# Kernel tuning notes

Hardware: AMD Instinct MI355X
Metric: run time of the kernel (lower is better)

## Reference

```python
import jax, jax.numpy as jnp
import numpy as np
from jax import lax

N = 64          # padded / uniform graph size
B = 512         # number of graph pairs
E = 512         # edges per graph
GCN_SIZES = [64, 32, 16]
CONV_OUT = [8, 16, 32]
D_IN = 16


def gcn_conv(x, src, dst, W, b):
    # PyG GCNConv: add self-loops, symmetric norm D^-1/2 (A+I) D^-1/2, then XW + b
    n = x.shape[0]
    h = x @ W
    deg = jnp.zeros((n,), x.dtype).at[dst].add(1.0) + 1.0  # +1 self-loop
    dinv = lax.rsqrt(deg)
    msg = h[src] * (dinv[src] * dinv[dst])[:, None]
    agg = jnp.zeros_like(h).at[dst].add(msg) + h * (dinv * dinv)[:, None]
    return agg + b


def gcn_pass(x, ei, Ws, bs):
    src, dst = ei[0], ei[1]
    feats = []
    h = x
    for i in range(len(Ws)):
        h = gcn_conv(h, src, dst, Ws[i], bs[i])
        feats.append(h)               # pre-ReLU features are used for similarity
        if i < len(Ws) - 1:
            h = jax.nn.relu(h)        # dropout p used in eval -> identity
    return feats


def conv_same(x, w, b):
    y = lax.conv_general_dilated(x, w, (1, 1), 'SAME',
                                 dimension_numbers=('NCHW', 'OIHW', 'NCHW'))
    return y + b[None, :, None, None]


def maxpool2(x):
    return lax.reduce_window(x, -jnp.inf, lax.max, (1, 1, 2, 2), (1, 1, 2, 2), 'VALID')


def setup_inputs() -> dict:
    key = jax.random.key(0)
    ks = jax.random.split(key, 32)
    f32 = jnp.float32
    x_q = jax.random.normal(ks[0], (B * N, D_IN), f32)
    x_c = jax.random.normal(ks[1], (B * N, D_IN), f32)
    off = (jnp.arange(B, dtype=jnp.int32) * N)[:, None]
    eq_s = (jax.random.randint(ks[2], (B, E), 0, N, jnp.int32) + off).reshape(-1)
    eq_d = (jax.random.randint(ks[3], (B, E), 0, N, jnp.int32) + off).reshape(-1)
    ec_s = (jax.random.randint(ks[4], (B, E), 0, N, jnp.int32) + off).reshape(-1)
    ec_d = (jax.random.randint(ks[5], (B, E), 0, N, jnp.int32) + off).reshape(-1)
    edge_q = jnp.stack([eq_s, eq_d])
    edge_c = jnp.stack([ec_s, ec_d])

    def lin(k, fi, fo):
        return jax.random.normal(k, (fi, fo), f32) / np.sqrt(fi)

    inp = dict(x_q=x_q, x_c=x_c, edge_q=edge_q, edge_c=edge_c)
    dims = [D_IN] + GCN_SIZES
    for i in range(3):
        inp[f'gcn_w{i+1}'] = lin(ks[6 + i], dims[i], dims[i + 1])
        inp[f'gcn_b{i+1}'] = jnp.zeros((dims[i + 1],), f32)
    cin = [1] + CONV_OUT[:-1]
    for i in range(3):
        fan = cin[i] * 25
        inp[f'conv_w{i+1}'] = jax.random.normal(ks[10 + i], (3, CONV_OUT[i], cin[i], 5, 5), f32) / np.sqrt(fan)
        inp[f'conv_b{i+1}'] = jnp.zeros((3, CONV_OUT[i]), f32)
    inp['lin_w1'] = lin(ks[14], 6144, 256)
    inp['lin_b1'] = jnp.zeros((256,), f32)
    inp['lin_w2'] = lin(ks[15], 256, 16)
    inp['lin_b2'] = jnp.zeros((16,), f32)
    inp['score_w'] = lin(ks[16], 16, 1)
    inp['score_b'] = jnp.zeros((1,), f32)
    return inp


def _forward(x_q, x_c, gcn_w1, gcn_b1, gcn_w2, gcn_b2, gcn_w3, gcn_b3,
             conv_w1, conv_b1, conv_w2, conv_b2, conv_w3, conv_b3,
             lin_w1, lin_b1, lin_w2, lin_b2, score_w, score_b,
             edge_q, edge_c):
    Ws = (gcn_w1, gcn_w2, gcn_w3)
    bs = (gcn_b1, gcn_b2, gcn_b3)
    qf = gcn_pass(x_q, edge_q, Ws, bs)   # list of [B*N, d_i]
    cf = gcn_pass(x_c, edge_c, Ws, bs)
    sims = [jnp.einsum('bnd,bmd->bnm', q.reshape(B, N, -1), c.reshape(B, N, -1))
            for q, c in zip(qf, cf)]
    cw = (conv_w1, conv_w2, conv_w3)
    cb = (conv_b1, conv_b2, conv_b3)
    outs = []
    for m in range(3):                    # separate conv weights per similarity matrix
        z = sims[m][:, None]              # [B, 1, N, N]
        for l in range(3):
            z = maxpool2(jax.nn.relu(conv_same(z, cw[l][m], cb[l][m])))
        outs.append(z)                    # [B, 32, 8, 8]
    feat = jnp.concatenate(outs, axis=1).reshape(B, 6144)
    h = jax.nn.relu(feat @ lin_w1 + lin_b1)
    h = jax.nn.relu(h @ lin_w2 + lin_b2)
    return (h @ score_w + score_b).reshape(-1)  # is_sig=False -> logits [B]


def reference(x_q, x_c, edge_q, edge_c, gcn_w1, gcn_b1, gcn_w2, gcn_b2, gcn_w3, gcn_b3,
              conv_w1, conv_b1, conv_w2, conv_b2, conv_w3, conv_b3,
              lin_w1, lin_b1, lin_w2, lin_b2, score_w, score_b):
    return _forward(x_q, x_c, gcn_w1, gcn_b1, gcn_w2, gcn_b2, gcn_w3, gcn_b3,
                    conv_w1, conv_b1, conv_w2, conv_b2, conv_w3, conv_b3,
                    lin_w1, lin_b1, lin_w2, lin_b2, score_w, score_b,
                    edge_q, edge_c)
```

## Files before the change

kernel.cpp:

```cpp
#include <hip/hip_runtime.h>
#include <hip/hip_bf16.h>

constexpr int B = 512, N = 64, E = 512, NE = B * E;

typedef __attribute__((ext_vector_type(8))) short bf8v;
typedef __attribute__((ext_vector_type(4))) float f32x4;
typedef unsigned short u16;

__device__ __forceinline__ u16 f2bf(float f) {
  unsigned u = __builtin_bit_cast(unsigned, f);
  u += 0x7FFFu + ((u >> 16) & 1u);
  return (u16)(u >> 16);
}

__device__ __forceinline__ int cmin(int a, int b) { return a < b ? a : b; }

template <int DIN, int DOUT, int NR, int NC, bool STORE_NEXT>
__device__ __forceinline__ void gcn_layer(
    float* __restrict__ At, float* __restrict__ Xt, float* __restrict__ Hs,
    const float* __restrict__ W, const float* __restrict__ bias,
    u16* __restrict__ fout, int g, int t) {
  constexpr int XS = 68;
  constexpr int CT = DOUT / NC;
  static_assert((64 / NR) * CT == 512, "thread mapping");
  const int ct = t % CT, nt = t / CT;
  const int n0 = NR * nt, c0 = NC * ct;
  {
    float acc[NR][NC] = {};
#pragma unroll 4
    for (int k = 0; k < DIN; ++k) {
      float xa[NR];
      if constexpr (NR == 4) {
        float4 xv = *(const float4*)&Xt[k * XS + n0];
        xa[0] = xv.x; xa[1] = xv.y; xa[2] = xv.z; xa[3] = xv.w;
      } else {
        float2 xv = *(const float2*)&Xt[k * XS + n0];
        xa[0] = xv.x; xa[1] = xv.y;
      }
      float wa[NC];
      if constexpr (NC == 2) {
        float2 wv = *(const float2*)&W[k * DOUT + c0];
        wa[0] = wv.x; wa[1] = wv.y;
      } else {
        wa[0] = W[k * DOUT + c0];
      }
#pragma unroll
      for (int i = 0; i < NR; ++i)
#pragma unroll
        for (int j = 0; j < NC; ++j) acc[i][j] += xa[i] * wa[j];
    }
#pragma unroll
    for (int i = 0; i < NR; ++i) {
      if constexpr (NC == 2)
        *(float2*)&Hs[(n0 + i) * XS + c0] = make_float2(acc[i][0], acc[i][1]);
      else
        Hs[(n0 + i) * XS + c0] = acc[i][0];
    }
  }
  __syncthreads();
  {
    float acc[NR][NC] = {};
#pragma unroll 4
    for (int s = 0; s < N; ++s) {
      float aa[NR];
      if constexpr (NR == 4) {
        float4 av = *(const float4*)&At[s * XS + n0];
        aa[0] = av.x; aa[1] = av.y; aa[2] = av.z; aa[3] = av.w;
      } else {
        float2 av = *(const float2*)&At[s * XS + n0];
        aa[0] = av.x; aa[1] = av.y;
      }
      float ha[NC];
      if constexpr (NC == 2) {
        float2 hv = *(const float2*)&Hs[s * XS + c0];
        ha[0] = hv.x; ha[1] = hv.y;
      } else {
        ha[0] = Hs[s * XS + c0];
      }
#pragma unroll
      for (int i = 0; i < NR; ++i)
#pragma unroll
        for (int j = 0; j < NC; ++j) acc[i][j] += aa[i] * ha[j];
    }
    float bv[NC];
#pragma unroll
    for (int j = 0; j < NC; ++j) bv[j] = bias[c0 + j];
#pragma unroll
    for (int i = 0; i < NR; ++i) {
      float st[NC];
#pragma unroll
      for (int j = 0; j < NC; ++j) st[j] = acc[i][j] + bv[j];
      if constexpr (NC == 2) {
        unsigned pack = (unsigned)f2bf(st[0]) | ((unsigned)f2bf(st[1]) << 16);
        *(unsigned*)&fout[(size_t)g * N * DOUT + (size_t)(n0 + i) * DOUT + c0] = pack;
      } else {
        fout[(size_t)g * N * DOUT + (size_t)(n0 + i) * DOUT + c0] = f2bf(st[0]);
      }
      if (STORE_NEXT) {
#pragma unroll
        for (int j = 0; j < NC; ++j)
          Xt[(c0 + j) * XS + n0 + i] = fmaxf(st[j], 0.f);
      }
    }
  }
  __syncthreads();
}

__global__ __launch_bounds__(512) void gcn_fused(
    const float* __restrict__ xq, const float* __restrict__ xc,
    const float* __restrict__ W1, const float* __restrict__ b1,
    const float* __restrict__ W2, const float* __restrict__ b2,
    const float* __restrict__ W3, const float* __restrict__ b3,
    const int* __restrict__ eq, const int* __restrict__ ec,
    u16* __restrict__ f1q, u16* __restrict__ f1c,
    u16* __restrict__ f2q, u16* __restrict__ f2c,
    u16* __restrict__ f3q, u16* __restrict__ f3c) {
  constexpr int XS = 68;
  __shared__ __align__(16) float At[N * XS];
  __shared__ __align__(16) float Xt[N * XS];
  __shared__ __align__(16) float Hs[N * XS];
  __shared__ float dl[N];
  __shared__ int cnt[N];
  const int g = blockIdx.x, t = threadIdx.x;
  const float* x = blockIdx.y ? xc : xq;
  const int* edges = blockIdx.y ? ec : eq;
  u16* o1 = blockIdx.y ? f1c : f1q;
  u16* o2 = blockIdx.y ? f2c : f2q;
  u16* o3 = blockIdx.y ? f3c : f3q;
  for (int i = t; i < N * 16; i += 512) {
    int n = i / 16, k = i % 16;
    Xt[k * XS + n] = x[(size_t)g * N * 16 + i];
  }
  for (int i = t; i < N * XS; i += 512) At[i] = 0.f;
  if (t < N) cnt[t] = 1;
  __syncthreads();
  const int* srcp = edges + (size_t)g * E;
  const int* dstp = edges + NE + (size_t)g * E;
  for (int j = t; j < E; j += 512) atomicAdd(&cnt[dstp[j] & 63], 1);
  __syncthreads();
  if (t < N) dl[t] = rsqrtf((float)cnt[t]);
  __syncthreads();
  for (int j = t; j < E; j += 512) {
    int s = srcp[j] & 63, d = dstp[j] & 63;
    atomicAdd(&At[s * XS + d], dl[s] * dl[d]);
  }
  if (t < N) atomicAdd(&At[t * XS + t], dl[t] * dl[t]);
  __syncthreads();
  gcn_layer<16, 64, 4, 2, true>(At, Xt, Hs, W1, b1, o1, g, t);
  gcn_layer<64, 32, 4, 1, true>(At, Xt, Hs, W2, b2, o2, g, t);
  gcn_layer<32, 16, 2, 1, false>(At, Xt, Hs, W3, b3, o3, g, t);
}

__global__ __launch_bounds__(256, 4) void simconv1(
    const u16* __restrict__ f1q, const u16* __restrict__ f1c,
    const u16* __restrict__ f2q, const u16* __restrict__ f2c,
    const u16* __restrict__ f3q, const u16* __restrict__ f3c,
    const float* __restrict__ w, const float* __restrict__ bias,
    u16* __restrict__ out) {
  constexpr int PS = 68, QS = 72;
  __shared__ __align__(16) u16 Qs[64 * QS];
  __shared__ __align__(16) u16 Cs[64 * QS];
  __shared__ __align__(16) float simp[68 * 68];
  __shared__ float wls[25 * 8];
  __shared__ float bls[8];
  const int b = blockIdx.x, m = blockIdx.y, t = threadIdx.x;
  for (int i = t; i < 68 * 68; i += 256) simp[i] = 0.f;
  if (t < 200) {
    int oc = t / 25, tap = t % 25;
    wls[tap * 8 + oc] = w[m * 200 + t];
  }
  if (t < 8) bls[t] = bias[m * 8 + t];
  const u16* fq = (m == 0) ? f1q : (m == 1) ? f2q : f3q;
  const u16* fc = (m == 0) ? f1c : (m == 1) ? f2c : f3c;
  const int D = 64 >> m;
  const int SEG = D >> 3;
  for (int i = t; i < 64 * SEG; i += 256) {
    int n = i / SEG, s = i - n * SEG;
    *(uint4*)&Qs[n * QS + s * 8] = *(const uint4*)&fq[(size_t)b * 64 * D + n * D + s * 8];
    *(uint4*)&Cs[n * QS + s * 8] = *(const uint4*)&fc[(size_t)b * 64 * D + n * D + s * 8];
  }
  if (m == 2 && t < 128) {
    int n = t >> 1, s = t & 1;
    uint4 z = {0u, 0u, 0u, 0u};
    *(uint4*)&Qs[n * QS + 16 + s * 8] = z;
    *(uint4*)&Cs[n * QS + 16 + s * 8] = z;
  }
  __syncthreads();
  const int w4 = t >> 6, lane = t & 63;
  const int r16 = lane & 15, kg = lane >> 4;
  const int Kpad = (m == 0) ? 64 : 32;
#pragma unroll 1
  for (int ct = 0; ct < 4; ++ct) {
    f32x4 acc = {0.f, 0.f, 0.f, 0.f};
    for (int ks = 0; ks < Kpad; ks += 32) {
      bf8v a = *(const bf8v*)&Qs[(w4 * 16 + r16) * QS + ks + kg * 8];
      bf8v bb = *(const bf8v*)&Cs[(ct * 16 + r16) * QS + ks + kg * 8];
      acc = __builtin_amdgcn_mfma_f32_16x16x32_bf16(a, bb, acc, 0, 0, 0);
    }
#pragma unroll
    for (int j = 0; j < 4; ++j)
      simp[(w4 * 16 + kg * 4 + j + 2) * PS + ct * 16 + r16 + 2] = acc[j];
  }
  __syncthreads();
  const int gy = t >> 4, gx = t & 15;
  float pr[8][8];
#pragma unroll
  for (int yy = 0; yy < 8; ++yy) {
    float4 a = *(const float4*)&simp[(4 * gy + yy) * PS + 4 * gx];
    float4 bb = *(const float4*)&simp[(4 * gy + yy) * PS + 4 * gx + 4];
    pr[yy][0] = a.x; pr[yy][1] = a.y; pr[yy][2] = a.z; pr[yy][3] = a.w;
    pr[yy][4] = bb.x; pr[yy][5] = bb.y; pr[yy][6] = bb.z; pr[yy][7] = bb.w;
  }
  u16* op = out + (size_t)(b * 3 + m) * 8192;
#pragma unroll 1
  for (int p2 = 0; p2 < 4; ++p2) {
    float acc[2][16];
#pragma unroll
    for (int p = 0; p < 16; ++p) { acc[0][p] = 0.f; acc[1][p] = 0.f; }
#pragma unroll
    for (int ky = 0; ky < 5; ++ky)
#pragma unroll
      for (int kx = 0; kx < 5; ++kx) {
        float2 wv = *(const float2*)&wls[(ky * 5 + kx) * 8 + p2 * 2];
#pragma unroll
        for (int dy = 0; dy < 4; ++dy)
#pragma unroll
          for (int dx = 0; dx < 4; ++dx) {
            float rv = pr[ky + dy][kx + dx];
            acc[0][dy * 4 + dx] += rv * wv.x;
            acc[1][dy * 4 + dx] += rv * wv.y;
          }
      }
    float b0 = bls[p2 * 2], b1 = bls[p2 * 2 + 1];
#pragma unroll
    for (int ay = 0; ay < 2; ++ay)
#pragma unroll
      for (int ax = 0; ax < 2; ++ax) {
        float v0 = fmaxf(fmaxf(acc[0][(2 * ay) * 4 + 2 * ax], acc[0][(2 * ay) * 4 + 2 * ax + 1]),
                         fmaxf(acc[0][(2 * ay + 1) * 4 + 2 * ax], acc[0][(2 * ay + 1) * 4 + 2 * ax + 1]));
        float v1 = fmaxf(fmaxf(acc[1][(2 * ay) * 4 + 2 * ax], acc[1][(2 * ay) * 4 + 2 * ax + 1]),
                         fmaxf(acc[1][(2 * ay + 1) * 4 + 2 * ax], acc[1][(2 * ay + 1) * 4 + 2 * ax + 1]));
        v0 = fmaxf(v0 + b0, 0.f);
        v1 = fmaxf(v1 + b1, 0.f);
        unsigned pack = (unsigned)f2bf(v0) | ((unsigned)f2bf(v1) << 16);
        *(unsigned*)&op[(size_t)(((2 * gy + ay) * 32) + (2 * gx + ax)) * 8 + p2 * 2] = pack;
      }
  }
}

__global__ __launch_bounds__(256) void prep_kernel(
    const float* __restrict__ lw1, const float* __restrict__ cw2,
    const float* __restrict__ cw3, u16* __restrict__ wT,
    u16* __restrict__ w2p, u16* __restrict__ w3p) {
  const int t = threadIdx.x;
  if (blockIdx.x < 384) {
    __shared__ float tile[64][65];
    const int k0 = (blockIdx.x % 96) * 64, c0 = (blockIdx.x / 96) * 64;
    for (int i = t; i < 4096; i += 256) {
      int r = i >> 6, c = i & 63;
      tile[r][c] = lw1[(size_t)(k0 + r) * 256 + c0 + c];
    }
    __syncthreads();
    for (int i = t; i < 4096; i += 256) {
      int c = i >> 6, k = i & 63;
      wT[(size_t)(c0 + c) * 6144 + k0 + k] = f2bf(tile[k][c]);
    }
    return;
  }
  int i = (blockIdx.x - 384) * 256 + t;
  if (i < 3 * 7 * 16 * 40) {
    int m = i / 4480, r = i % 4480;
    int k = r % 40, rest = r / 40, oc = rest & 15, st = rest >> 4;
    u16 v = 0;
    if (k < 32) {
      int sl = k >> 3, ci = k & 7, tap = st * 4 + sl;
      if (tap < 25) v = f2bf(cw2[((size_t)(m * 16 + oc) * 8 + ci) * 25 + tap]);
    }
    w2p[i] = v;
  }
  if (i < 3 * 26 * 16 * 40) {
    int m = i / 16640, r = i % 16640;
    int k = r % 40, rest = r / 40, oc16 = rest & 15, sthalf = rest >> 4;
    int half = sthalf & 1, st = sthalf >> 1;
    u16 v = 0;
    if (k < 32) {
      int sl = k >> 4, ci = k & 15, tap = st * 2 + sl;
      int oc = half * 16 + oc16;
      if (tap < 25) v = f2bf(cw3[((size_t)(m * 32 + oc) * 16 + ci) * 25 + tap]);
    }
    w3p[i] = v;
  }
}

__global__ __launch_bounds__(256) void conv2_mfma(
    const u16* __restrict__ in, const u16* __restrict__ w2p,
    const float* __restrict__ bias, u16* __restrict__ out) {
  constexpr int PW = 36, BS = 40;
  __shared__ __align__(16) u16 ins[PW * PW * 8];
  __shared__ __align__(16) u16 wls[7 * 16 * BS];
  __shared__ float bls[16];
  const int b = blockIdx.x, m = blockIdx.y, t = threadIdx.x;
  const size_t ibase = (size_t)(b * 3 + m) * 8192;
  for (int i = t; i < PW * PW; i += 256) {
    int y = i / PW, x = i % PW;
    uint4 v = {0u, 0u, 0u, 0u};
    if (y >= 2 && y < 34 && x >= 2 && x < 34)
      v = *(const uint4*)&in[ibase + (size_t)((y - 2) * 32 + (x - 2)) * 8];
    *(uint4*)&ins[i * 8] = v;
  }
  {
    const u16* wsrc = w2p + m * 4480;
    for (int i = t; i < 560; i += 256) *(uint4*)&wls[i * 8] = *(const uint4*)&wsrc[i * 8];
  }
  if (t < 16) bls[t] = bias[m * 16 + t];
  __syncthreads();
  const int wv = t >> 6, lane = t & 63;
  const int oc = lane & 15, g = lane >> 4;
  const int xt = wv & 1, ypb = wv >> 1;
  const int x = xt * 16 + oc;
  const size_t obase = (size_t)(b * 3 + m) * 4096;
#pragma unroll 1
  for (int grp = 0; grp < 2; ++grp) {
    f32x4 acc[4][2];
#pragma unroll
    for (int i = 0; i < 4; ++i) {
      acc[i][0] = (f32x4){0.f, 0.f, 0.f, 0.f};
      acc[i][1] = (f32x4){0.f, 0.f, 0.f, 0.f};
    }
#pragma unroll
    for (int st = 0; st < 7; ++st) {
      bf8v bvv = *(const bf8v*)&wls[(st * 16 + oc) * BS + g * 8];
      const int c0 = cmin(st * 4 + 0, 24), c1 = cmin(st * 4 + 1, 24);
      const int c2 = cmin(st * 4 + 2, 24), c3 = cmin(st * 4 + 3, 24);
      const int k0 = (c0 / 5) * PW + c0 % 5, k1 = (c1 / 5) * PW + c1 % 5;
      const int k2 = (c2 / 5) * PW + c2 % 5, k3 = (c3 / 5) * PW + c3 % 5;
      const int koff = (g == 0) ? k0 : (g == 1) ? k1 : (g == 2) ? k2 : k3;
#pragma unroll
      for (int i = 0; i < 4; ++i) {
        const int y0 = 2 * ypb + 4 * (grp * 4 + i);
        const int abase = (y0 * PW + x + koff) * 8;
        bf8v a0 = *(const bf8v*)&ins[abase];
        acc[i][0] = __builtin_amdgcn_mfma_f32_16x16x32_bf16(a0, bvv, acc[i][0], 0, 0, 0);
        bf8v a1 = *(const bf8v*)&ins[abase + PW * 8];
        acc[i][1] = __builtin_amdgcn_mfma_f32_16x16x32_bf16(a1, bvv, acc[i][1], 0, 0, 0);
      }
    }
    const float bb = bls[oc];
#pragma unroll
    for (int i = 0; i < 4; ++i) {
      const int yp = ypb + 2 * (grp * 4 + i);
      const float v0 = fmaxf(fmaxf(fmaxf(acc[i][0][0], acc[i][0][1]),
                                   fmaxf(acc[i][1][0], acc[i][1][1])) + bb, 0.f);
      const float v1 = fmaxf(fmaxf(fmaxf(acc[i][0][2], acc[i][0][3]),
                                   fmaxf(acc[i][1][2], acc[i][1][3])) + bb, 0.f);
      const int px = xt * 8 + 2 * g;
      out[obase + (size_t)((yp * 16 + px) * 16 + oc)] = f2bf(v0);
      out[obase + (size_t)((yp * 16 + px + 1) * 16 + oc)] = f2bf(v1);
    }
  }
}

__global__ __launch_bounds__(256) void conv3_mfma(
    const u16* __restrict__ in, const u16* __restrict__ w3p,
    const float* __restrict__ bias, u16* __restrict__ feat) {
  constexpr int PW = 20, BS = 40;
  __shared__ __align__(16) u16 ins[PW * PW * 16];
  __shared__ __align__(16) u16 wls[26 * 16 * BS];
  __shared__ float bls[32];
  const int b = blockIdx.x, m = blockIdx.y, t = threadIdx.x;
  const size_t ibase = (size_t)(b * 3 + m) * 4096;
  for (int i = t; i < PW * PW; i += 256) {
    int y = i / PW, x = i % PW;
    uint4 v0 = {0u, 0u, 0u, 0u}, v1 = {0u, 0u, 0u, 0u};
    if (y >= 2 && y < 18 && x >= 2 && x < 18) {
      const u16* p = &in[ibase + (size_t)((y - 2) * 16 + (x - 2)) * 16];
      v0 = *(const uint4*)p;
      v1 = *(const uint4*)(p + 8);
    }
    *(uint4*)&ins[i * 16] = v0;
    *(uint4*)&ins[i * 16 + 8] = v1;
  }
  {
    const u16* wsrc = w3p + m * 16640;
    for (int i = t; i < 2080; i += 256) *(uint4*)&wls[i * 8] = *(const uint4*)&wsrc[i * 8];
  }
  if (t < 32) bls[t] = bias[m * 32 + t];
  __syncthreads();
  const int wv = t >> 6, lane = t & 63;
  const int oc = lane & 15, g = lane >> 4;
  const int sl = g >> 1, ch = (g & 1) * 8;
  const int half = wv & 1, ypb = wv >> 1;
  u16* fb = feat + (size_t)b * 6144 + m * 2048;
  f32x4 acc[4][2];
#pragma unroll
  for (int i = 0; i < 4; ++i) {
    acc[i][0] = (f32x4){0.f, 0.f, 0.f, 0.f};
    acc[i][1] = (f32x4){0.f, 0.f, 0.f, 0.f};
  }
#pragma unroll
  for (int st = 0; st < 13; ++st) {
    bf8v bvv = *(const bf8v*)&wls[(size_t)((st * 2 + half) * 16 + oc) * BS + g * 8];
    const int c0 = cmin(st * 2 + 0, 24), c1 = cmin(st * 2 + 1, 24);
    const int k0 = (c0 / 5) * PW + c0 % 5, k1 = (c1 / 5) * PW + c1 % 5;
    const int koff = sl ? k1 : k0;
#pragma unroll
    for (int i = 0; i < 4; ++i) {
      const int y0 = 2 * ypb + 4 * i;
      const int abase = (y0 * PW + oc + koff) * 16 + ch;
      bf8v a0 = *(const bf8v*)&ins[abase];
      acc[i][0] = __builtin_amdgcn_mfma_f32_16x16x32_bf16(a0, bvv, acc[i][0], 0, 0, 0);
      bf8v a1 = *(const bf8v*)&ins[abase + PW * 16];
      acc[i][1] = __builtin_amdgcn_mfma_f32_16x16x32_bf16(a1, bvv, acc[i][1], 0, 0, 0);
    }
  }
  const int ocg = half * 16 + oc;
  const float bb = bls[ocg];
#pragma unroll
  for (int i = 0; i < 4; ++i) {
    const int yp = ypb + 2 * i;
    const float v0 = fmaxf(fmaxf(fmaxf(acc[i][0][0], acc[i][0][1]),
                                 fmaxf(acc[i][1][0], acc[i][1][1])) + bb, 0.f);
    const float v1 = fmaxf(fmaxf(fmaxf(acc[i][0][2], acc[i][0][3]),
                                 fmaxf(acc[i][1][2], acc[i][1][3])) + bb, 0.f);
    unsigned pack = (unsigned)f2bf(v0) | ((unsigned)f2bf(v1) << 16);
    *(unsigned*)&fb[ocg * 64 + yp * 8 + 2 * g] = pack;
  }
}

__global__ __launch_bounds__(256) void lin1_mfma(const u16* __restrict__ feat,
                                                 const u16* __restrict__ wT,
                                                 float* __restrict__ h1p) {
  constexpr int AS = 72;
  __shared__ __align__(16) u16 As[64 * AS];
  __shared__ __align__(16) u16 Bs[64 * AS];
  const int r0 = blockIdx.x * 64, c0 = blockIdx.y * 64, kb = blockIdx.z * 384;
  const int t = threadIdx.x;
  const int w = t >> 6, lane = t & 63;
  const int row16 = lane & 15, kg = lane >> 4;
  f32x4 acc[4] = {{0.f, 0.f, 0.f, 0.f}, {0.f, 0.f, 0.f, 0.f},
                  {0.f, 0.f, 0.f, 0.f}, {0.f, 0.f, 0.f, 0.f}};
  const int lr = t >> 2, lk = (t & 3) * 16;
#pragma unroll 1
  for (int st = 0; st < 6; ++st) {
    __syncthreads();
    const int ks = kb + st * 64;
    {
      const u16* srcA = feat + (size_t)(r0 + lr) * 6144 + ks + lk;
      uint4 a0 = *(const uint4*)srcA;
      uint4 a1 = *(const uint4*)(srcA + 8);
      *(uint4*)&As[lr * AS + lk] = a0;
      *(uint4*)&As[lr * AS + lk + 8] = a1;
      const u16* srcB = wT + (size_t)(c0 + lr) * 6144 + ks + lk;
      uint4 b0 = *(const uint4*)srcB;
      uint4 b1 = *(const uint4*)(srcB + 8);
      *(uint4*)&Bs[lr * AS + lk] = b0;
      *(uint4*)&Bs[lr * AS + lk + 8] = b1;
    }
    __syncthreads();
#pragma unroll
    for (int kk = 0; kk < 2; ++kk) {
      bf8v a = *(const bf8v*)&As[(w * 16 + row16) * AS + kk * 32 + kg * 8];
#pragma unroll
      for (int ct = 0; ct < 4; ++ct) {
        bf8v bb = *(const bf8v*)&Bs[(ct * 16 + row16) * AS + kk * 32 + kg * 8];
        acc[ct] = __builtin_amdgcn_mfma_f32_16x16x32_bf16(a, bb, acc[ct], 0, 0, 0);
      }
    }
  }
  float* out = h1p + (size_t)blockIdx.z * 131072;
#pragma unroll
  for (int ct = 0; ct < 4; ++ct)
#pragma unroll
    for (int j = 0; j < 4; ++j)
      out[(size_t)(r0 + w * 16 + kg * 4 + j) * 256 + c0 + ct * 16 + row16] = acc[ct][j];
}

__global__ __launch_bounds__(256) void head_kernel(
    const float* __restrict__ h1p, const float* __restrict__ b1,
    const float* __restrict__ w2, const float* __restrict__ b2,
    const float* __restrict__ sw, const float* __restrict__ sb,
    float* __restrict__ out) {
  constexpr int HS = 260;
  __shared__ __align__(16) float h1s[16 * HS];
  __shared__ __align__(16) float w2s[256 * 16];
  const int r0 = blockIdx.x * 16, t = threadIdx.x;
  for (int i = t; i < 4096; i += 256) {
    int r = i >> 8, k = i & 255;
    float s = b1[k];
#pragma unroll
    for (int p = 0; p < 16; ++p) s += h1p[(size_t)p * 131072 + (size_t)(r0 + r) * 256 + k];
    h1s[r * HS + k] = s;
    w2s[i] = w2[i];
  }
  __syncthreads();
  const int j = t & 15, r = t >> 4;
  float acc = b2[j];
#pragma unroll 4
  for (int k4 = 0; k4 < 64; ++k4) {
    float4 hv = *(const float4*)&h1s[r * HS + 4 * k4];
    float h0 = fmaxf(hv.x, 0.f), h1v = fmaxf(hv.y, 0.f);
    float h2v = fmaxf(hv.z, 0.f), h3 = fmaxf(hv.w, 0.f);
    acc += h0 * w2s[(4 * k4 + 0) * 16 + j];
    acc += h1v * w2s[(4 * k4 + 1) * 16 + j];
    acc += h2v * w2s[(4 * k4 + 2) * 16 + j];
    acc += h3 * w2s[(4 * k4 + 3) * 16 + j];
  }
  float v = fmaxf(acc, 0.f) * sw[j];
#pragma unroll
  for (int off = 8; off; off >>= 1) v += __shfl_xor(v, off, 16);
  if (j == 0) out[r0 + r] = v + sb[0];
}

extern "C" void kernel_launch(void* const* d_in, const int* in_sizes, int n_in,
                              void* d_out, int out_size, void* d_ws, size_t ws_size,
                              hipStream_t stream) {
  const float* x_q = (const float*)d_in[0];
  const float* x_c = (const float*)d_in[1];
  const int* edge_q = (const int*)d_in[2];
  const int* edge_c = (const int*)d_in[3];
  const float* gw1 = (const float*)d_in[4];
  const float* gb1 = (const float*)d_in[5];
  const float* gw2 = (const float*)d_in[6];
  const float* gb2 = (const float*)d_in[7];
  const float* gw3 = (const float*)d_in[8];
  const float* gb3 = (const float*)d_in[9];
  const float* cw1 = (const float*)d_in[10];
  const float* cb1 = (const float*)d_in[11];
  const float* cw2 = (const float*)d_in[12];
  const float* cb2 = (const float*)d_in[13];
  const float* cw3 = (const float*)d_in[14];
  const float* cb3 = (const float*)d_in[15];
  const float* lw1 = (const float*)d_in[16];
  const float* lb1 = (const float*)d_in[17];
  const float* lw2 = (const float*)d_in[18];
  const float* lb2 = (const float*)d_in[19];
  const float* swt = (const float*)d_in[20];
  const float* sbs = (const float*)d_in[21];
  float* ws = (float*)d_ws;

  const size_t o_f1q = 65536;
  const size_t o_f2q = o_f1q + 2097152;
  const size_t o_f3q = o_f2q + 1048576;
  const size_t o_f1c = o_f3q + 524288;
  const size_t o_f2c = o_f1c + 2097152;
  const size_t o_f3c = o_f2c + 1048576;
  const size_t o_sims = o_f3c + 524288;
  const size_t o_pm1 = o_sims + 6291456;
  const size_t o_pm2 = o_pm1 + 6291456;
  const size_t o_wT = o_pm2 + 3145728;
  const size_t o_w2p = o_wT + 786432;
  const size_t o_w3p = o_w2p + 8192;
  const size_t o_feat = o_sims;
  const size_t o_h1p = o_f1q;

  u16* f1q = (u16*)(ws + o_f1q); u16* f2q = (u16*)(ws + o_f2q); u16* f3q = (u16*)(ws + o_f3q);
  u16* f1c = (u16*)(ws + o_f1c); u16* f2c = (u16*)(ws + o_f2c); u16* f3c = (u16*)(ws + o_f3c);
  u16* pm1 = (u16*)(ws + o_pm1);
  u16* pm2 = (u16*)(ws + o_pm2);
  u16* wT = (u16*)(ws + o_wT);
  u16* w2p = (u16*)(ws + o_w2p);
  u16* w3p = (u16*)(ws + o_w3p);
  u16* feat = (u16*)(ws + o_feat);
  float* h1p = ws + o_h1p;

  prep_kernel<<<580, 256, 0, stream>>>(lw1, cw2, cw3, wT, w2p, w3p);

  gcn_fused<<<dim3(B, 2), 512, 0, stream>>>(x_q, x_c, gw1, gb1, gw2, gb2, gw3, gb3,
                                            edge_q, edge_c, f1q, f1c, f2q, f2c, f3q, f3c);

  simconv1<<<dim3(B, 3), 256, 0, stream>>>(f1q, f1c, f2q, f2c, f3q, f3c, cw1, cb1, pm1);

  conv2_mfma<<<dim3(B, 3), 256, 0, stream>>>(pm1, w2p, cb2, pm2);
  conv3_mfma<<<dim3(B, 3), 256, 0, stream>>>(pm2, w3p, cb3, feat);

  lin1_mfma<<<dim3(8, 4, 16), 256, 0, stream>>>(feat, wT, h1p);
  head_kernel<<<32, 256, 0, stream>>>(h1p, lb1, lw2, lb2, swt, sbs, (float*)d_out);
}
```

Baseline: 136.7 us.

## Fuse conv2 and conv3 into one kernel keeping pooled activations in LDS

Merges the conv2 and conv3 MFMA kernels into a single kernel per (batch, matrix) block. The pooled conv2 output is written straight into a zero-padded shared-memory tile that conv3 reads, so the pm2 round trip through global memory and one kernel launch go away. Conv3 weights are loaded into a shared buffer reused from the conv2 input region after a barrier. The cost is higher per-block LDS use, which may lower occupancy, plus extra barriers and a serialized weight load between the two stages.

```diff
diff --git a/kernel.cpp b/kernel.cpp
--- a/kernel.cpp
+++ b/kernel.cpp
@@ -292,35 +292,92 @@
   }
 }
 
-__global__ __launch_bounds__(256) void conv2_mfma(
+__global__ __launch_bounds__(256) void conv23_mfma(
     const u16* __restrict__ in, const u16* __restrict__ w2p,
-    const float* __restrict__ bias, u16* __restrict__ out) {
-  constexpr int PW = 36, BS = 40;
-  __shared__ __align__(16) u16 ins[PW * PW * 8];
-  __shared__ __align__(16) u16 wls[7 * 16 * BS];
-  __shared__ float bls[16];
+    const float* __restrict__ cb2, const u16* __restrict__ w3p,
+    const float* __restrict__ cb3, u16* __restrict__ feat) {
+  constexpr int PW2 = 36, PW3 = 20, BS = 40;
+  __shared__ __align__(16) u16 uni[16640];
+  __shared__ __align__(16) u16 p2s[PW3 * PW3 * 16];
+  __shared__ float bls2[16];
+  __shared__ float bls3[32];
   const int b = blockIdx.x, m = blockIdx.y, t = threadIdx.x;
+  u16* ins2 = uni;
+  u16* w2ls = uni + 10368;
   const size_t ibase = (size_t)(b * 3 + m) * 8192;
-  for (int i = t; i < PW * PW; i += 256) {
-    int y = i / PW, x = i % PW;
+  for (int i = t; i < PW2 * PW2; i += 256) {
+    int y = i / PW2, x = i % PW2;
     uint4 v = {0u, 0u, 0u, 0u};
     if (y >= 2 && y < 34 && x >= 2 && x < 34)
       v = *(const uint4*)&in[ibase + (size_t)((y - 2) * 32 + (x - 2)) * 8];
-    *(uint4*)&ins[i * 8] = v;
+    *(uint4*)&ins2[i * 8] = v;
   }
   {
     const u16* wsrc = w2p + m * 4480;
-    for (int i = t; i < 560; i += 256) *(uint4*)&wls[i * 8] = *(const uint4*)&wsrc[i * 8];
-  }
-  if (t < 16) bls[t] = bias[m * 16 + t];
+    for (int i = t; i < 560; i += 256) *(uint4*)&w2ls[i * 8] = *(const uint4*)&wsrc[i * 8];
+  }
+  {
+    uint4 z = {0u, 0u, 0u, 0u};
+    for (int i = t; i < 800; i += 256) *(uint4*)&p2s[i * 8] = z;
+  }
+  if (t < 16) bls2[t] = cb2[m * 16 + t];
+  if (t >= 32 && t < 64) bls3[t - 32] = cb3[m * 32 + (t - 32)];
   __syncthreads();
   const int wv = t >> 6, lane = t & 63;
   const int oc = lane & 15, g = lane >> 4;
-  const int xt = wv & 1, ypb = wv >> 1;
-  const int x = xt * 16 + oc;
-  const size_t obase = (size_t)(b * 3 + m) * 4096;
+  {
+    const int xt = wv & 1, ypb = wv >> 1;
+    const int x = xt * 16 + oc;
 #pragma unroll 1
-  for (int grp = 0; grp < 2; ++grp) {
+    for (int grp = 0; grp < 2; ++grp) {
+      f32x4 acc[4][2];
+#pragma unroll
+      for (int i = 0; i < 4; ++i) {
+        acc[i][0] = (f32x4){0.f, 0.f, 0.f, 0.f};
+        acc[i][1] = (f32x4){0.f, 0.f, 0.f, 0.f};
+      }
+#pragma unroll
+      for (int st = 0; st < 7; ++st) {
+        bf8v bvv = *(const bf8v*)&w2ls[(st * 16 + oc) * BS + g * 8];
+        const int c0 = cmin(st * 4 + 0, 24), c1 = cmin(st * 4 + 1, 24);
+        const int c2 = cmin(st * 4 + 2, 24), c3 = cmin(st * 4 + 3, 24);
+        const int k0 = (c0 / 5) * PW2 + c0 % 5, k1 = (c1 / 5) * PW2 + c1 % 5;
+        const int k2 = (c2 / 5) * PW2 + c2 % 5, k3 = (c3 / 5) * PW2 + c3 % 5;
+        const int koff = (g == 0) ? k0 : (g == 1) ? k1 : (g == 2) ? k2 : k3;
+#pragma unroll
+        for (int i = 0; i < 4; ++i) {
+          const int y0 = 2 * ypb + 4 * (grp * 4 + i);
+          const int abase = (y0 * PW2 + x + koff) * 8;
+          bf8v a0 = *(const bf8v*)&ins2[abase];
+          acc[i][0] = __builtin_amdgcn_mfma_f32_16x16x32_bf16(a0, bvv, acc[i][0], 0, 0, 0);
+          bf8v a1 = *(const bf8v*)&ins2[abase + PW2 * 8];
+          acc[i][1] = __builtin_amdgcn_mfma_f32_16x16x32_bf16(a1, bvv, acc[i][1], 0, 0, 0);
+        }
+      }
+      const float bb = bls2[oc];
+#pragma unroll
+      for (int i = 0; i < 4; ++i) {
+        const int yp = ypb + 2 * (grp * 4 + i);
+        const float v0 = fmaxf(fmaxf(fmaxf(acc[i][0][0], acc[i][0][1]),
+                                     fmaxf(acc[i][1][0], acc[i][1][1])) + bb, 0.f);
+        const float v1 = fmaxf(fmaxf(fmaxf(acc[i][0][2], acc[i][0][3]),
+                                     fmaxf(acc[i][1][2], acc[i][1][3])) + bb, 0.f);
+        const int px = xt * 8 + 2 * g;
+        p2s[((yp + 2) * PW3 + (px + 2)) * 16 + oc] = f2bf(v0);
+        p2s[((yp + 2) * PW3 + (px + 3)) * 16 + oc] = f2bf(v1);
+      }
+    }
+  }
+  __syncthreads();
+  {
+    const u16* wsrc = w3p + m * 16640;
+    for (int i = t; i < 2080; i += 256) *(uint4*)&uni[i * 8] = *(const uint4*)&wsrc[i * 8];
+  }
+  __syncthreads();
+  {
+    const int sl = g >> 1, ch = (g & 1) * 8;
+    const int half = wv & 1, ypb = wv >> 1;
+    u16* fb = feat + (size_t)b * 6144 + m * 2048;
     f32x4 acc[4][2];
 #pragma unroll
     for (int i = 0; i < 4; ++i) {
@@ -328,102 +385,33 @@
       acc[i][1] = (f32x4){0.f, 0.f, 0.f, 0.f};
     }
 #pragma unroll
-    for (int st = 0; st < 7; ++st) {
-      bf8v bvv = *(const bf8v*)&wls[(st * 16 + oc) * BS + g * 8];
-      const int c0 = cmin(st * 4 + 0, 24), c1 = cmin(st * 4 + 1, 24);
-      const int c2 = cmin(st * 4 + 2, 24), c3 = cmin(st * 4 + 3, 24);
-      const int k0 = (c0 / 5) * PW + c0 % 5, k1 = (c1 / 5) * PW + c1 % 5;
-      const int k2 = (c2 / 5) * PW + c2 % 5, k3 = (c3 / 5) * PW + c3 % 5;
-      const int koff = (g == 0) ? k0 : (g == 1) ? k1 : (g == 2) ? k2 : k3;
+    for (int st = 0; st < 13; ++st) {
+      bf8v bvv = *(const bf8v*)&uni[(size_t)((st * 2 + half) * 16 + oc) * BS + g * 8];
+      const int c0 = cmin(st * 2 + 0, 24), c1 = cmin(st * 2 + 1, 24);
+      const int k0 = (c0 / 5) * PW3 + c0 % 5, k1 = (c1 / 5) * PW3 + c1 % 5;
+      const int koff = sl ? k1 : k0;
 #pragma unroll
       for (int i = 0; i < 4; ++i) {
-        const int y0 = 2 * ypb + 4 * (grp * 4 + i);
-        const int abase = (y0 * PW + x + koff) * 8;
-        bf8v a0 = *(const bf8v*)&ins[abase];
+        const int y0 = 2 * ypb + 4 * i;
+        const int abase = (y0 * PW3 + oc + koff) * 16 + ch;
+        bf8v a0 = *(const bf8v*)&p2s[abase];
         acc[i][0] = __builtin_amdgcn_mfma_f32_16x16x32_bf16(a0, bvv, acc[i][0], 0, 0, 0);
-        bf8v a1 = *(const bf8v*)&ins[abase + PW * 8];
+        bf8v a1 = *(const bf8v*)&p2s[abase + PW3 * 16];
         acc[i][1] = __builtin_amdgcn_mfma_f32_16x16x32_bf16(a1, bvv, acc[i][1], 0, 0, 0);
       }
     }
-    const float bb = bls[oc];
+    const int ocg = half * 16 + oc;
+    const float bb = bls3[ocg];
 #pragma unroll
     for (int i = 0; i < 4; ++i) {
-      const int yp = ypb + 2 * (grp * 4 + i);
+      const int yp = ypb + 2 * i;
       const float v0 = fmaxf(fmaxf(fmaxf(acc[i][0][0], acc[i][0][1]),
                                    fmaxf(acc[i][1][0], acc[i][1][1])) + bb, 0.f);
       const float v1 = fmaxf(fmaxf(fmaxf(acc[i][0][2], acc[i][0][3]),
                                    fmaxf(acc[i][1][2], acc[i][1][3])) + bb, 0.f);
-      const int px = xt * 8 + 2 * g;
-      out[obase + (size_t)((yp * 16 + px) * 16 + oc)] = f2bf(v0);
-      out[obase + (size_t)((yp * 16 + px + 1) * 16 + oc)] = f2bf(v1);
-    }
-  }
-}
-
-__global__ __launch_bounds__(256) void conv3_mfma(
-    const u16* __restrict__ in, const u16* __restrict__ w3p,
-    const float* __restrict__ bias, u16* __restrict__ feat) {
-  constexpr int PW = 20, BS = 40;
-  __shared__ __align__(16) u16 ins[PW * PW * 16];
-  __shared__ __align__(16) u16 wls[26 * 16 * BS];
-  __shared__ float bls[32];
-  const int b = blockIdx.x, m = blockIdx.y, t = threadIdx.x;
-  const size_t ibase = (size_t)(b * 3 + m) * 4096;
-  for (int i = t; i < PW * PW; i += 256) {
-    int y = i / PW, x = i % PW;
-    uint4 v0 = {0u, 0u, 0u, 0u}, v1 = {0u, 0u, 0u, 0u};
-    if (y >= 2 && y < 18 && x >= 2 && x < 18) {
-      const u16* p = &in[ibase + (size_t)((y - 2) * 16 + (x - 2)) * 16];
-      v0 = *(const uint4*)p;
-      v1 = *(const uint4*)(p + 8);
-    }
-    *(uint4*)&ins[i * 16] = v0;
-    *(uint4*)&ins[i * 16 + 8] = v1;
-  }
-  {
-    const u16* wsrc = w3p + m * 16640;
-    for (int i = t; i < 2080; i += 256) *(uint4*)&wls[i * 8] = *(const uint4*)&wsrc[i * 8];
-  }
-  if (t < 32) bls[t] = bias[m * 32 + t];
-  __syncthreads();
-  const int wv = t >> 6, lane = t & 63;
-  const int oc = lane & 15, g = lane >> 4;
-  const int sl = g >> 1, ch = (g & 1) * 8;
-  const int half = wv & 1, ypb = wv >> 1;
-  u16* fb = feat + (size_t)b * 6144 + m * 2048;
-  f32x4 acc[4][2];
-#pragma unroll
-  for (int i = 0; i < 4; ++i) {
-    acc[i][0] = (f32x4){0.f, 0.f, 0.f, 0.f};
-    acc[i][1] = (f32x4){0.f, 0.f, 0.f, 0.f};
-  }
-#pragma unroll
-  for (int st = 0; st < 13; ++st) {
-    bf8v bvv = *(const bf8v*)&wls[(size_t)((st * 2 + half) * 16 + oc) * BS + g * 8];
-    const int c0 = cmin(st * 2 + 0, 24), c1 = cmin(st * 2 + 1, 24);
-    const int k0 = (c0 / 5) * PW + c0 % 5, k1 = (c1 / 5) * PW + c1 % 5;
-    const int koff = sl ? k1 : k0;
-#pragma unroll
-    for (int i = 0; i < 4; ++i) {
-      const int y0 = 2 * ypb + 4 * i;
-      const int abase = (y0 * PW + oc + koff) * 16 + ch;
-      bf8v a0 = *(const bf8v*)&ins[abase];
-      acc[i][0] = __builtin_amdgcn_mfma_f32_16x16x32_bf16(a0, bvv, acc[i][0], 0, 0, 0);
-      bf8v a1 = *(const bf8v*)&ins[abase + PW * 16];
-      acc[i][1] = __builtin_amdgcn_mfma_f32_16x16x32_bf16(a1, bvv, acc[i][1], 0, 0, 0);
-    }
-  }
-  const int ocg = half * 16 + oc;
-  const float bb = bls[ocg];
-#pragma unroll
-  for (int i = 0; i < 4; ++i) {
-    const int yp = ypb + 2 * i;
-    const float v0 = fmaxf(fmaxf(fmaxf(acc[i][0][0], acc[i][0][1]),
-                                 fmaxf(acc[i][1][0], acc[i][1][1])) + bb, 0.f);
-    const float v1 = fmaxf(fmaxf(fmaxf(acc[i][0][2], acc[i][0][3]),
-                                 fmaxf(acc[i][1][2], acc[i][1][3])) + bb, 0.f);
-    unsigned pack = (unsigned)f2bf(v0) | ((unsigned)f2bf(v1) << 16);
-    *(unsigned*)&fb[ocg * 64 + yp * 8 + 2 * g] = pack;
+      unsigned pack = (unsigned)f2bf(v0) | ((unsigned)f2bf(v1) << 16);
+      *(unsigned*)&fb[ocg * 64 + yp * 8 + 2 * g] = pack;
+    }
   }
 }
 
@@ -556,7 +544,6 @@
   u16* f1q = (u16*)(ws + o_f1q); u16* f2q = (u16*)(ws + o_f2q); u16* f3q = (u16*)(ws + o_f3q);
   u16* f1c = (u16*)(ws + o_f1c); u16* f2c = (u16*)(ws + o_f2c); u16* f3c = (u16*)(ws + o_f3c);
   u16* pm1 = (u16*)(ws + o_pm1);
-  u16* pm2 = (u16*)(ws + o_pm2);
   u16* wT = (u16*)(ws + o_wT);
   u16* w2p = (u16*)(ws + o_w2p);
   u16* w3p = (u16*)(ws + o_w3p);
@@ -570,8 +557,7 @@
 
   simconv1<<<dim3(B, 3), 256, 0, stream>>>(f1q, f1c, f2q, f2c, f3q, f3c, cw1, cb1, pm1);
 
-  conv2_mfma<<<dim3(B, 3), 256, 0, stream>>>(pm1, w2p, cb2, pm2);
-  conv3_mfma<<<dim3(B, 3), 256, 0, stream>>>(pm2, w3p, cb3, feat);
+  conv23_mfma<<<dim3(B, 3), 256, 0, stream>>>(pm1, w2p, cb2, w3p, cb3, feat);
 
   lin1_mfma<<<dim3(8, 4, 16), 256, 0, stream>>>(feat, wT, h1p);
   head_kernel<<<32, 256, 0, stream>>>(h1p, lb1, lw2, lb2, swt, sbs, (float*)d_out);
```

Result: faster. 131.1 us (-4.1%).
